# Kernel optimization log

Measured on AMD Instinct MI355X. Metric: run time of the kernel, lower is better.

The kernel has to match this reference:

```python
import jax, jax.numpy as jnp
import numpy as np

N = 100000      # nodes
E = 3200000     # edges
H = 64          # node_hidden_dim
DIN = 15        # node_input_dim
DOUT = 12       # output_dim
NT = 5          # num_edge_type
G = 256         # graphs in batch
STEPS = 6       # num_step_prop


def setup_inputs() -> dict:
    key = jax.random.key(0)
    ks = jax.random.split(key, 24)
    s = 0.1
    n = lambda k, shp: jax.random.normal(k, shp, jnp.float32) * s
    return {
        "x": jax.random.normal(ks[0], (N, DIN), jnp.float32),
        "edge_index": jax.random.randint(ks[1], (2, E), 0, N, dtype=jnp.int32),
        "edge_attr": jax.random.randint(ks[2], (E,), 0, NT, dtype=jnp.int32),
        "batch": jnp.sort(jax.random.randint(ks[3], (N,), 0, G, dtype=jnp.int32)),
        "lin0_w": n(ks[4], (DIN, H)), "lin0_b": n(ks[5], (H,)),
        "edge_embed": n(ks[6], (NT, H * H)),
        "conv_bias": n(ks[7], (H,)),
        "gru_w_ih": n(ks[8], (H, 3 * H)), "gru_w_hh": n(ks[9], (H, 3 * H)),
        "gru_b_ih": n(ks[10], (3 * H,)), "gru_b_hh": n(ks[11], (3 * H,)),
        "i_w1": n(ks[12], (2 * H, H)), "i_b1": n(ks[13], (H,)),
        "i_w2": n(ks[14], (H, DOUT)), "i_b2": n(ks[15], (DOUT,)),
        "j_w1": n(ks[16], (H, H)), "j_b1": n(ks[17], (H,)),
        "j_w2": n(ks[18], (H, DOUT)), "j_b2": n(ks[19], (DOUT,)),
    }


def reference(x, edge_index, edge_attr, batch,
              lin0_w, lin0_b, edge_embed, conv_bias,
              gru_w_ih, gru_w_hh, gru_b_ih, gru_b_hh,
              i_w1, i_b1, i_w2, i_b2, j_w1, j_b1, j_w2, j_b2):
    src, dst = edge_index[0], edge_index[1]
    W_types = edge_embed.reshape(NT, H, H)  # per edge-type [H_in, H_out]

    # in-degree for mean aggregation (PyG: isolated nodes get 0)
    deg = jax.ops.segment_sum(jnp.ones((E,), x.dtype), dst, num_segments=N)
    deg = jnp.maximum(deg, 1.0)[:, None]

    out0 = jax.nn.relu(x @ lin0_w + lin0_b)
    out = out0
    h = out0

    for _ in range(STEPS):
        # NNConv: per-edge matmul m_e = x_src[e] @ W[type_e].
        # Only NT=5 edge types exist -> precompute all 5 transforms, then gather.
        T = jnp.einsum('nh,tho->nto', out, W_types)        # [N, NT, H]
        msg = T[src, edge_attr]                            # [E, H] gather
        agg = jax.ops.segment_sum(msg, dst, num_segments=N) / deg + conv_bias
        m = jax.nn.relu(agg)

        # GRU cell (torch gate order: r, z, n)
        gx = m @ gru_w_ih + gru_b_ih
        gh = h @ gru_w_hh + gru_b_hh
        xr, xz, xn = jnp.split(gx, 3, axis=1)
        hr, hz, hn = jnp.split(gh, 3, axis=1)
        r = jax.nn.sigmoid(xr + hr)
        z = jax.nn.sigmoid(xz + hz)
        nn_ = jnp.tanh(xn + r * hn)
        h = (1.0 - z) * nn_ + z * h
        out = h

    # gated readout
    i = jax.nn.sigmoid(
        jax.nn.sigmoid(jnp.concatenate([out, out0], axis=1) @ i_w1 + i_b1) @ i_w2 + i_b2)
    j = jax.nn.sigmoid(out @ j_w1 + j_b1) @ j_w2 + j_b2
    gated = i * j                                          # [N, DOUT]
    return jax.ops.segment_sum(gated, batch, num_segments=G)  # [G, DOUT]
```

## Files before the change

kernel.cpp:

```cpp
#include <hip/hip_runtime.h>
#include <hip/hip_bf16.h>

typedef __hip_bfloat16 bf16;
using short8 = __attribute__((ext_vector_type(8))) short;
using f32x4  = __attribute__((ext_vector_type(4))) float;
using f32x2  = __attribute__((ext_vector_type(2))) float;

#define MFMA16(a,b,c) __builtin_amdgcn_mfma_f32_16x16x32_bf16((a),(b),(c),0,0,0)
#define MAXBUCK 4096
#define SB 72
#define MSTR 72
#define SRCCAP 1024
#define CHK 8192
#define MAXNC 512
#define BCAP 2816

__device__ __forceinline__ float b2f(bf16 v){ return __bfloat162float(v); }
__device__ __forceinline__ bf16  f2b(float v){ return __float2bfloat16(v); }
__device__ __forceinline__ float sigmf(float x){ return 1.f/(1.f+__expf(-x)); }
__device__ __forceinline__ float tanhfast(float x){
  x = fminf(fmaxf(x,-15.f),15.f);
  float e = __expf(2.f*x);
  return (e-1.f)/(e+1.f);
}
__device__ __forceinline__ short8 ld_frag(const bf16* p){
  return *reinterpret_cast<const short8*>(p);
}
__device__ __forceinline__ short f2bits(float f){
  unsigned u = __builtin_bit_cast(unsigned, f);
  unsigned r = (u + 0x7FFFu + ((u>>16)&1u)) >> 16;
  return (short)r;
}
__device__ __forceinline__ f32x2 pk_add(f32x2 a, f32x2 b){
  f32x2 d;
  asm("v_pk_add_f32 %0, %1, %2" : "=v"(d) : "v"(a), "v"(b));
  return d;
}
__device__ __forceinline__ unsigned cvtpk_bf16(float lo, float hi){
  unsigned r;
  asm("v_cvt_pk_bf16_f32 %0, %1, %2" : "=v"(r) : "v"(lo), "v"(hi));
  return r;
}

__device__ __forceinline__ f32x2 cvt8lo(unsigned w){
  f32x2 r;
  asm("v_cvt_pk_f32_fp8 %0, %1" : "=v"(r) : "v"(w));
  return r;
}
__device__ __forceinline__ f32x2 cvt8hi(unsigned w){
  return cvt8lo(w >> 16);
}
__device__ __forceinline__ unsigned short f32pair_to_fp8(float a, float b){
  unsigned r = 0;
  asm("v_cvt_pk_fp8_f32 %0, %1, %2" : "+v"(r) : "v"(a), "v"(b));
  return (unsigned short)(r & 0xffffu);
}

__global__ void k_sniff(const unsigned int* __restrict__ x, int* __restrict__ flag,
      int* __restrict__ bkt_cnt, int nb,
      int* __restrict__ s0, int* __restrict__ s1,
      int* __restrict__ s2, int* __restrict__ s3){
  int t = threadIdx.x;
  if (blockIdx.x == 1){
    for (int i=t;i<nb;i+=256) bkt_cnt[i]=0;
    return;
  }
  if (blockIdx.x == 2){
    if (t<32){ s0[t]=0; s1[t]=0; }
    if (t<16){ s2[t]=0; s3[t]=0; }
    return;
  }
  int good = 0;
  for (int i=t; i<4096; i+=256){
    unsigned w = x[i];
    unsigned e = (w>>23)&0xFFu;
    unsigned m = w & 0x7FFFFFFFu;
    if ((e>=100u && e<=150u) || m==0u) good++;
  }
  __shared__ int sm[256];
  sm[t]=good; __syncthreads();
  if (t==0){ int s=0; for (int k=0;k<256;k++) s+=sm[k]; *flag = (s>2048)?1:0; }
}

struct PtrPack { const void* p[17]; };

#define CAN_X     0
#define CAN_L0W   1500032
#define CAN_L0B   1500992
#define CAN_EE    1501056
#define CAN_CB    1521536
#define CAN_WIH   1521600
#define CAN_WHH   1533888
#define CAN_BIH   1546176
#define CAN_BHH   1546368
#define CAN_IW1   1546560
#define CAN_IB1   1554752
#define CAN_IW2   1554816
#define CAN_IB2   1555584
#define CAN_JW1   1555648
#define CAN_JB1   1559744
#define CAN_JW2   1559808
#define CAN_JB2   1560576
#define CAN_TOT   1560640

__global__ void k_canon(PtrPack pk, const int* __restrict__ flag, bf16* __restrict__ dst){
  static const int offs[17] = {CAN_X,CAN_L0W,CAN_L0B,CAN_EE,CAN_CB,CAN_WIH,CAN_WHH,
    CAN_BIH,CAN_BHH,CAN_IW1,CAN_IB1,CAN_IW2,CAN_IB2,CAN_JW1,CAN_JB1,CAN_JW2,CAN_JB2};
  static const int szs[17]  = {1500000,960,64,20480,64,12288,12288,192,192,8192,64,768,12,4096,64,768,12};
  int t = blockIdx.x*256+threadIdx.x;
  if (t >= CAN_TOT) return;
  int s = 0;
  #pragma unroll
  for (int k=1;k<17;k++) if (t >= offs[k]) s = k;
  int i = t - offs[s];
  float v = 0.f;
  if (i < szs[s]){
    if (*flag) v = ((const float*)pk.p[s])[i];
    else       v = b2f(((const bf16*)pk.p[s])[i]);
  }
  dst[t] = f2b(v);
}


__global__ __launch_bounds__(1024) void k_scan(const int* __restrict__ cnt, int n,
      int* __restrict__ ptr, int* __restrict__ cursor){
  __shared__ int ws[17];
  int tid = threadIdx.x, lane = tid&63, w = tid>>6;
  int run = 0;
  for (int base=0; base<n; base+=1024){
    int i = base + tid;
    int v = (i<n)? cnt[i] : 0;
    int incl = v;
    #pragma unroll
    for (int off=1; off<64; off<<=1){
      int t = __shfl_up(incl, off, 64);
      if (lane>=off) incl += t;
    }
    if (lane==63) ws[w] = incl;
    __syncthreads();
    if (tid==0){ int r=0; for (int k=0;k<16;k++){ int t=ws[k]; ws[k]=r; r+=t; } ws[16]=r; }
    __syncthreads();
    int excl = run + ws[w] + incl - v;
    if (i<n){
      ptr[i] = excl;
      if (cursor) cursor[i] = excl;
    }
    run += ws[16];
    __syncthreads();
  }
  if (tid==0) ptr[n] = run;
}

__global__ __launch_bounds__(512) void k_csort(const int* __restrict__ srcv,
      const int* __restrict__ dstv, const int* __restrict__ eav, int E_, int nb, int NC,
      unsigned int* __restrict__ bucketed, int* __restrict__ rs, int* __restrict__ bkt_cnt){
  __shared__ int lh[MAXBUCK];
  __shared__ int lofs[MAXBUCK];
  __shared__ int ws[9];
  int c = blockIdx.x, tid = threadIdx.x;
  int base = c*CHK, end = min(base+CHK, E_);
  for (int i=tid;i<nb;i+=512) lh[i]=0;
  __syncthreads();
  for (int i=base+tid; i<end; i+=512) atomicAdd(&lh[dstv[i]>>5], 1);
  __syncthreads();
  int lane=tid&63, w=tid>>6;
  int run=0;
  for (int bb=0; bb<nb; bb+=512){
    int i=bb+tid;
    int v=(i<nb)? lh[i]:0;
    int incl=v;
    #pragma unroll
    for (int off=1;off<64;off<<=1){
      int t=__shfl_up(incl,off,64);
      if (lane>=off) incl+=t;
    }
    if (lane==63) ws[w]=incl;
    __syncthreads();
    if (tid==0){ int r=0; for(int k=0;k<8;k++){int t=ws[k];ws[k]=r;r+=t;} ws[8]=r; }
    __syncthreads();
    if (i<nb) lofs[i]= run + ws[w] + incl - v;
    run += ws[8];
    __syncthreads();
  }
  for (int i=tid;i<nb;i+=512){
    rs[(size_t)i*NC + c] = base + lofs[i];
    int cntv = lh[i];
    if (cntv) atomicAdd(&bkt_cnt[i], cntv);
  }
  if (tid==0) rs[(size_t)nb*NC + c] = end;
  __syncthreads();
  for (int i=base+tid;i<end;i+=512){
    int d = dstv[i];
    int bin = d>>5;
    int pos = base + atomicAdd(&lofs[bin], 1);
    bucketed[pos] = (((unsigned)((d&31)*5 + eav[i]))<<17) | (unsigned)srcv[i];
  }
}

__global__ __launch_bounds__(256) void k_bsort2(const unsigned int* __restrict__ bucketed,
      const int* __restrict__ rs, int NC,
      const int* __restrict__ bkt_ptr, int nb, int E_,
      int* __restrict__ kptr, int* __restrict__ sorted_src,
      unsigned char* __restrict__ kperm){
  __shared__ unsigned sbuf[BCAP];
  __shared__ int rofs[MAXNC+1];
  __shared__ int rstart[MAXNC];
  __shared__ int scan2[2][MAXNC];
  __shared__ int cnt[160], sc[160], cur[160];
  int b = blockIdx.x, tid = threadIdx.x;
  int s = bkt_ptr[b], e = bkt_ptr[b+1];
  int size = e - s;
  const int* rowA = rs + (size_t)b*NC;
  const int* rowB = rs + (size_t)(b+1)*NC;
  bool fits = (NC <= MAXNC);
  if (fits){
    for (int i=tid; i<MAXNC; i+=256){
      int v = 0;
      if (i < NC){
        int a = rowA[i];
        rstart[i] = a;
        v = rowB[i] - a;
      }
      scan2[0][i] = v;
    }
    __syncthreads();
    int pp = 0;
    #pragma unroll
    for (int off=1; off<MAXNC; off<<=1){
      for (int i=tid; i<MAXNC; i+=256){
        int nv = scan2[pp][i];
        if (i>=off) nv += scan2[pp][i-off];
        scan2[pp^1][i] = nv;
      }
      __syncthreads();
      pp ^= 1;
    }
    if (tid==0) rofs[0]=0;
    for (int i=tid; i<NC; i+=256) rofs[i+1] = scan2[pp][i];
    __syncthreads();
  }
  bool staged = fits && (size <= BCAP);
  if (staged){
    for (int i=tid; i<size; i+=256){
      int lo=0, hi=NC-1;
      while (lo<hi){ int mid=(lo+hi+1)>>1; if (rofs[mid]<=i) lo=mid; else hi=mid-1; }
      sbuf[i] = bucketed[rstart[lo] + (i - rofs[lo])];
    }
  }
  __syncthreads();
  if (tid<160) cnt[tid]=0;
  __syncthreads();
  if (staged){
    for (int i=tid;i<size;i+=256) atomicAdd(&cnt[sbuf[i]>>17], 1);
  } else {
    for (int c2=0;c2<NC;c2++){
      int st=rowA[c2], ln=rowB[c2]-st;
      for (int k=tid;k<ln;k+=256) atomicAdd(&cnt[bucketed[st+k]>>17], 1);
    }
  }
  __syncthreads();
  if (tid<160) sc[tid]=cnt[tid];
  __syncthreads();
  #pragma unroll
  for (int off=1; off<160; off<<=1){
    int v = 0;
    if (tid<160 && tid>=off) v = sc[tid-off];
    __syncthreads();
    if (tid<160) sc[tid] += v;
    __syncthreads();
  }
  if (tid<160){
    int basek = s + sc[tid] - cnt[tid];
    kptr[b*160+tid] = basek;
    cur[tid] = basek;
  }
  if (b==nb-1 && tid==0) kptr[(size_t)nb*160] = e;
  if (tid<160){
    int hbase = (tid<80)? 0 : 80;
    int me = cnt[tid];
    int r = 0;
    for (int j=0;j<80;j++){
      int jj = hbase+j;
      int cj = cnt[jj];
      r += (cj>me) || (cj==me && jj<tid);
    }
    kperm[((size_t)b*2 + (tid<80?0:1))*80 + r] = (unsigned char)(tid - hbase);
  }
  __syncthreads();
  if (staged){
    for (int i=tid;i<size;i+=256){
      unsigned p = sbuf[i];
      int pos = atomicAdd(&cur[p>>17], 1);
      sorted_src[pos] = (int)(p & 0x1FFFFu);
    }
  } else {
    for (int c2=0;c2<NC;c2++){
      int st=rowA[c2], ln=rowB[c2]-st;
      for (int k=tid;k<ln;k+=256){
        unsigned p = bucketed[st+k];
        int pos = atomicAdd(&cur[p>>17], 1);
        sorted_src[pos] = (int)(p & 0x1FFFFu);
      }
    }
  }
}

__global__ __launch_bounds__(256) void k_lin0(const bf16* __restrict__ x,
      const bf16* __restrict__ w, const bf16* __restrict__ b,
      bf16* __restrict__ out0, bf16* __restrict__ h,
      unsigned char* __restrict__ hq, int N_){
  int idx = blockIdx.x*256+threadIdx.x;
  int n = idx>>6, o = idx&63;
  if (n>=N_) return;
  float acc = b2f(b[o]);
  #pragma unroll
  for (int k=0;k<15;k++) acc += b2f(x[n*15+k]) * b2f(w[k*64+o]);
  float hv = fmaxf(acc,0.f);
  bf16 v = f2b(hv);
  out0[idx]=v; h[idx]=v;
  float hvn = __shfl_xor(hv, 1);
  if (!(o&1)) *(unsigned short*)(hq + (size_t)n*64 + o) = f32pair_to_fp8(hv, hvn);
}

__device__ __forceinline__ void d_swz(const unsigned short* src, int KS, int NC,
                                      unsigned short* dst, int nfrag, int t){
  if (t >= nfrag*64) return;
  int lane=t&63, frag=t>>6, cb=frag/KS, ks=frag%KS;
  int c = cb*16 + (lane&15);
  #pragma unroll
  for (int j=0;j<8;j++){
    int k = ks*32 + ((lane>>4)<<3) + j;
    dst[t*8+j] = (c<NC)? src[k*NC+c] : (unsigned short)0;
  }
}

__global__ __launch_bounds__(256) void k_prep(const bf16* __restrict__ ee,
      const bf16* __restrict__ wih, const bf16* __restrict__ whh,
      const bf16* __restrict__ iw1, const bf16* __restrict__ jw1,
      const bf16* __restrict__ iw2, const bf16* __restrict__ jw2,
      unsigned short* __restrict__ wall, unsigned short* __restrict__ wgru,
      unsigned short* __restrict__ wr1, unsigned short* __restrict__ wiw2s,
      unsigned short* __restrict__ wjw2s,
      const int* __restrict__ batch, int N_, int G_, int* __restrict__ gptr){
  int blk = blockIdx.x, tid = threadIdx.x;
  if (blk < 10){
    int t = blk*256+tid;
    if (t<2560){
      int lane=t&63, frag=t>>6, ct=frag/10, ks=frag%10;
      int c = ct*16 + (lane&15);
      #pragma unroll
      for (int j=0;j<8;j++){
        int k = ks*32 + ((lane>>4)<<3) + j;
        int tt = k>>6, kc = k&63;
        wall[t*8+j] = ((const unsigned short*)ee)[tt*4096 + kc*64 + c];
      }
    }
  } else if (blk < 16){
    d_swz((const unsigned short*)wih, 2, 192, wgru, 24, (blk-10)*256+tid);
  } else if (blk < 22){
    d_swz((const unsigned short*)whh, 2, 192, wgru+12288, 24, (blk-16)*256+tid);
  } else if (blk < 26){
    d_swz((const unsigned short*)iw1, 4, 64, wr1, 16, (blk-22)*256+tid);
  } else if (blk < 28){
    d_swz((const unsigned short*)jw1, 2, 64, wr1+8192, 8, (blk-26)*256+tid);
  } else if (blk == 28){
    d_swz((const unsigned short*)iw2, 2, 12, wiw2s, 2, tid);
  } else if (blk == 29){
    d_swz((const unsigned short*)jw2, 2, 12, wjw2s, 2, tid);
  } else {
    int g = (blk-30)*256+tid;
    if (g <= G_){
      int lo=0, hi=N_;
      while (lo<hi){ int mid=(lo+hi)>>1; if (batch[mid] < g) lo=mid+1; else hi=mid; }
      gptr[g]=lo;
    }
  }
}

__global__ __launch_bounds__(256,8) void k_step(const bf16* __restrict__ hin,
      bf16* __restrict__ hout,
      const unsigned char* __restrict__ hqin, unsigned char* __restrict__ hqout,
      const int* __restrict__ sorted_src, const int* __restrict__ kptr,
      const unsigned char* __restrict__ kperm,
      const unsigned short* __restrict__ wall, const unsigned short* __restrict__ wgru,
      const bf16* __restrict__ conv_bias, const bf16* __restrict__ bih,
      const bf16* __restrict__ bhh, int N_){
  __shared__ unsigned short Sb[80*SB];
  __shared__ int kp[81];
  __shared__ unsigned char pm[80];
  __shared__ char ubuf[SRCCAP*4 + 32];
  int* srcL = (int*)ubuf;
  unsigned short* m_s = (unsigned short*)ubuf;
  int tid=threadIdx.x, lane=tid&63, w=tid>>6;
  int b=blockIdx.x;
  if (tid<81) kp[tid]=kptr[(size_t)b*80+tid];
  if (tid<80) pm[tid]=kperm[(size_t)b*80+tid];
  __syncthreads();
  int s0g = kp[0];
  int elen = kp[80]-s0g;
  int cap = (elen<=SRCCAP)? elen : 0;
  for (int i=tid;i<cap;i+=256) srcL[i]=sorted_src[s0g+i]<<6;
  __syncthreads();
  int g=lane>>3, c=lane&7;
  const unsigned char* hp8 = hqin + (c<<3);
  const int sent = N_<<6;

  auto run_phase1 = [&](auto GET){
    #pragma unroll 1
    for (int jo=0;jo<5;jo++){
      int pbase = jo*16 + w*4;
      int p  = pm[pbase + (g&3)];
      int p0 = pm[pbase];
      int st = kp[p]-s0g, len = kp[p+1]-kp[p];
      int maxLen = kp[p0+1]-kp[p0];
      int sub = g>>2;
      f32x2 a01={0.f,0.f}, a23={0.f,0.f}, a45={0.f,0.f}, a67={0.f,0.f};
      for (int base=0; base<maxLen; base+=8){
        uint2 hv[4];
        #pragma unroll
        for (int u=0;u<4;u++){
          int idx = base + sub*4 + u;
          int s = GET(st+idx);
          s = (idx < len)? s : sent;
          hv[u] = *(const uint2*)(hp8 + (size_t)s);
        }
        #pragma unroll
        for (int u=0;u<4;u++){
          a01 = pk_add(a01, cvt8lo(hv[u].x));
          a23 = pk_add(a23, cvt8hi(hv[u].x));
          a45 = pk_add(a45, cvt8lo(hv[u].y));
          a67 = pk_add(a67, cvt8hi(hv[u].y));
        }
      }
      float a[8] = {a01.x,a01.y,a23.x,a23.y,a45.x,a45.y,a67.x,a67.y};
      #pragma unroll
      for (int j=0;j<8;j++) a[j] += __shfl_xor(a[j], 32);
      if (g<4){
        uint4 v;
        v.x = cvtpk_bf16(a[0],a[1]);
        v.y = cvtpk_bf16(a[2],a[3]);
        v.z = cvtpk_bf16(a[4],a[5]);
        v.w = cvtpk_bf16(a[6],a[7]);
        *reinterpret_cast<uint4*>(&Sb[(size_t)p*SB + c*8]) = v;
      }
    }
  };
  if (cap) run_phase1([&](int rel){ return srcL[rel]; });
  else     run_phase1([&](int rel){ return sorted_src[s0g+rel]<<6; });
  __syncthreads();

  int q=lane>>4, mr=lane&15;
  {
    int ct = w;
    f32x4 acc={0.f,0.f,0.f,0.f};
    #pragma unroll
    for (int ks=0;ks<10;ks++){
      int k0 = ks*32 + q*8;
      int tt = k0>>6, ch = k0&63;
      short8 af = *reinterpret_cast<const short8*>(&Sb[(size_t)(mr*5+tt)*SB + ch]);
      short8 bfrag = *(const short8*)(wall + (size_t)((ct*10+ks)*64+lane)*8);
      acc = MFMA16(af, bfrag, acc);
    }
    int col = ct*16+mr;
    float bi = b2f(conv_bias[col]);
    #pragma unroll
    for (int r=0;r<4;r++){
      int nl = q*4+r;
      int deg = kp[nl*5+5]-kp[nl*5];
      float dv = 1.f/fmaxf((float)deg,1.f);
      m_s[nl*MSTR+col] = (unsigned short)f2bits(fmaxf(acc[r]*dv+bi,0.f));
    }
  }
  __syncthreads();

  {
    int cc = w;
    int na = b*16+mr; if (na>N_-1) na=N_-1;
    short8 am0 = *(const short8*)(&m_s[mr*MSTR + q*8]);
    short8 am1 = *(const short8*)(&m_s[mr*MSTR + 32 + q*8]);
    short8 ah0 = ld_frag(hin + (size_t)na*64 + q*8);
    short8 ah1 = ld_frag(hin + (size_t)na*64 + 32 + q*8);
    const short8* Bw = reinterpret_cast<const short8*>(wgru);
    f32x4 xr={0.f,0.f,0.f,0.f}, xz=xr, xn=xr, hr=xr, hz=xr, hn=xr;
    xr = MFMA16(am0, Bw[((cc  )*2+0)*64+lane], xr);
    xr = MFMA16(am1, Bw[((cc  )*2+1)*64+lane], xr);
    xz = MFMA16(am0, Bw[((cc+4)*2+0)*64+lane], xz);
    xz = MFMA16(am1, Bw[((cc+4)*2+1)*64+lane], xz);
    xn = MFMA16(am0, Bw[((cc+8)*2+0)*64+lane], xn);
    xn = MFMA16(am1, Bw[((cc+8)*2+1)*64+lane], xn);
    hr = MFMA16(ah0, Bw[(24+(cc  )*2+0)*64+lane], hr);
    hr = MFMA16(ah1, Bw[(24+(cc  )*2+1)*64+lane], hr);
    hz = MFMA16(ah0, Bw[(24+(cc+4)*2+0)*64+lane], hz);
    hz = MFMA16(ah1, Bw[(24+(cc+4)*2+1)*64+lane], hz);
    hn = MFMA16(ah0, Bw[(24+(cc+8)*2+0)*64+lane], hn);
    hn = MFMA16(ah1, Bw[(24+(cc+8)*2+1)*64+lane], hn);
    int col = cc*16+mr;
    float bxr=b2f(bih[col]), bxz=b2f(bih[col+64]), bxn=b2f(bih[col+128]);
    float bhr=b2f(bhh[col]), bhz=b2f(bhh[col+64]), bhn=b2f(bhh[col+128]);
    #pragma unroll
    for (int r=0;r<4;r++){
      int row = q*4+r;
      int n = b*16+row;
      int nc = (n<N_)? n : N_-1;
      float rg = sigmf(xr[r]+bxr + hr[r]+bhr);
      float zg = sigmf(xz[r]+bxz + hz[r]+bhz);
      float ng = tanhfast(xn[r]+bxn + rg*(hn[r]+bhn));
      float ho = b2f(hin[(size_t)nc*64+col]);
      float hv = (1.f-zg)*ng + zg*ho;
      float hvn = __shfl_xor(hv, 1);
      if (n < N_){
        hout[(size_t)n*64+col] = f2b(hv);
        if (!(mr&1))
          *(unsigned short*)(hqout + (size_t)n*64 + col) = f32pair_to_fp8(hv, hvn);
      }
    }
  }
}

__global__ __launch_bounds__(256) void k_read(const bf16* __restrict__ h, const bf16* __restrict__ out0,
      const unsigned short* __restrict__ W, const bf16* __restrict__ ib1, const bf16* __restrict__ jb1,
      const unsigned short* __restrict__ iw2swz, const unsigned short* __restrict__ jw2swz,
      const bf16* __restrict__ ib2, const bf16* __restrict__ jb2,
      float* __restrict__ gated, int N_){
  __shared__ unsigned short lds[12288];
  __shared__ unsigned short sbuf[64*72];
  __shared__ unsigned short tbuf[64*72];
  { const int* s=(const int*)W; int* d=(int*)lds;
    for (int i=threadIdx.x;i<6144;i+=256) d[i]=s[i]; }
  __syncthreads();
  int tid=threadIdx.x, lane=tid&63, w=tid>>6, q=lane>>4;
  int nb = blockIdx.x*64 + w*16;
  int ar = nb + (lane&15); if (ar>N_-1) ar=N_-1;
  short8 ah0 = ld_frag(h + (size_t)ar*64 + q*8),    ah1 = ld_frag(h + (size_t)ar*64 + 32 + q*8);
  short8 ao0 = ld_frag(out0 + (size_t)ar*64 + q*8), ao1 = ld_frag(out0 + (size_t)ar*64 + 32 + q*8);
  const short8* Bi = reinterpret_cast<const short8*>(lds);
  const short8* Bj = reinterpret_cast<const short8*>(lds + 8192);
  int colb = lane&15;
  for (int cb=0; cb<4; cb++){
    f32x4 ai = {0.f,0.f,0.f,0.f};
    ai = MFMA16(ah0, Bi[(cb*4+0)*64+lane], ai);
    ai = MFMA16(ah1, Bi[(cb*4+1)*64+lane], ai);
    ai = MFMA16(ao0, Bi[(cb*4+2)*64+lane], ai);
    ai = MFMA16(ao1, Bi[(cb*4+3)*64+lane], ai);
    f32x4 aj = {0.f,0.f,0.f,0.f};
    aj = MFMA16(ah0, Bj[(cb*2+0)*64+lane], aj);
    aj = MFMA16(ah1, Bj[(cb*2+1)*64+lane], aj);
    int col = cb*16 + colb;
    float bi=b2f(ib1[col]), bj=b2f(jb1[col]);
    #pragma unroll
    for (int r=0;r<4;r++){
      int lrow = w*16 + q*4 + r;
      sbuf[lrow*72+col] = (unsigned short)f2bits(sigmf(ai[r]+bi));
      tbuf[lrow*72+col] = (unsigned short)f2bits(sigmf(aj[r]+bj));
    }
  }
  __syncthreads();
  int mr = lane&15;
  short8 as0 = *(const short8*)(&sbuf[(w*16+mr)*72 + q*8]);
  short8 as1 = *(const short8*)(&sbuf[(w*16+mr)*72 + 32 + q*8]);
  short8 at0 = *(const short8*)(&tbuf[(w*16+mr)*72 + q*8]);
  short8 at1 = *(const short8*)(&tbuf[(w*16+mr)*72 + 32 + q*8]);
  const short8* Bi2 = reinterpret_cast<const short8*>(iw2swz);
  const short8* Bj2 = reinterpret_cast<const short8*>(jw2swz);
  f32x4 ai = {0.f,0.f,0.f,0.f};
  ai = MFMA16(as0, Bi2[lane], ai);
  ai = MFMA16(as1, Bi2[64+lane], ai);
  f32x4 aj = {0.f,0.f,0.f,0.f};
  aj = MFMA16(at0, Bj2[lane], aj);
  aj = MFMA16(at1, Bj2[64+lane], aj);
  int col = lane&15;
  if (col<12){
    float bi=b2f(ib2[col]), bj=b2f(jb2[col]);
    #pragma unroll
    for (int r=0;r<4;r++){
      int row = nb + q*4 + r;
      if (row < N_) gated[(size_t)row*12+col] = sigmf(ai[r]+bi)*(aj[r]+bj);
    }
  }
}

__global__ __launch_bounds__(256) void k_graphsum(const float* __restrict__ gated,
      const int* __restrict__ gptr, const int* __restrict__ flag, void* __restrict__ outp){
  int g = blockIdx.x;
  int s = gptr[g], e = gptr[g+1];
  int tid = threadIdx.x;
  int c = tid & 15, rg = tid >> 4;
  float acc = 0.f;
  if (c < 12)
    for (int row = s + rg; row < e; row += 16) acc += gated[(size_t)row*12 + c];
  __shared__ float sm[256];
  sm[tid] = acc;
  __syncthreads();
  if (rg == 0 && c < 12){
    float t = 0.f;
    for (int k=0;k<16;k++) t += sm[k*16 + c];
    if (*flag) ((float*)outp)[g*12 + c] = t;
    else       ((bf16*) outp)[g*12 + c] = f2b(t);
  }
}


extern "C" void kernel_launch(void* const* d_in, const int* in_sizes, int n_in,
                              void* d_out, int out_size, void* d_ws, size_t ws_size,
                              hipStream_t stream){
  const int*  ei    = (const int*) d_in[1];
  const int*  ea    = (const int*) d_in[2];
  const int*  batch = (const int*) d_in[3];

  const int N_ = in_sizes[3];
  const int E_ = in_sizes[2];
  const int G_ = out_size / 12;
  const int nb  = (N_ + 31) >> 5;
  const int nbs = (N_ + 15) >> 4;
  const int NC  = (E_ + CHK - 1) / CHK;

  char* ws = (char*)d_ws;
  size_t off = 0;
  auto alloc = [&](size_t bytes)->size_t{
    size_t o = off; off += (bytes + 255) & ~(size_t)255; return o;
  };

  size_t oOut0   = alloc((size_t)N_*64*2);
  size_t oH0     = alloc((size_t)(N_+1)*64*2);
  size_t oH1     = alloc((size_t)(N_+1)*64*2);
  size_t oHq0    = alloc((size_t)(N_+1)*64);
  size_t oHq1    = alloc((size_t)(N_+1)*64);
  size_t oGated  = alloc((size_t)N_*12*4);
  size_t oBEdges = alloc((size_t)E_*4);
  size_t oSorted = alloc((size_t)E_*4 + 256);
  size_t oRS     = alloc((size_t)(nb+1)*NC*4);
  size_t oKptr   = alloc(((size_t)nb*160+2)*4);
  size_t oKperm  = alloc((size_t)nb*160);
  size_t oCanon  = alloc((size_t)CAN_TOT*2);
  size_t oCnt    = alloc((size_t)nb*4);
  size_t oBPtr   = alloc((size_t)(nb+1)*4);
  size_t oGptr   = alloc((size_t)(G_+1)*4);
  size_t oFlag   = alloc(256);
  size_t oWall   = alloc((size_t)20480*2);
  size_t oWgru   = alloc((size_t)24576*2);
  size_t oWr1    = alloc((size_t)12288*2);
  size_t oWiw2   = alloc((size_t)1024*2);
  size_t oWjw2   = alloc((size_t)1024*2);

  bf16*  out0    = (bf16*)(ws + oOut0);
  bf16*  h0      = (bf16*)(ws + oH0);
  bf16*  h1      = (bf16*)(ws + oH1);
  unsigned char* hq0 = (unsigned char*)(ws + oHq0);
  unsigned char* hq1 = (unsigned char*)(ws + oHq1);
  float* gated   = (float*)(ws + oGated);
  unsigned int* bucketed = (unsigned int*)(ws + oBEdges);
  int*   sorted_src = (int*)(ws + oSorted);
  int*   rs      = (int*)(ws + oRS);
  int*   kptr    = (int*)(ws + oKptr);
  unsigned char* kperm = (unsigned char*)(ws + oKperm);
  bf16*  can     = (bf16*)(ws + oCanon);
  int*   bkt_cnt = (int*)(ws + oCnt);
  int*   bkt_ptr = (int*)(ws + oBPtr);
  int*   gptr    = (int*)(ws + oGptr);
  int*   flag    = (int*)(ws + oFlag);
  unsigned short* wall  = (unsigned short*)(ws + oWall);
  unsigned short* wgru  = (unsigned short*)(ws + oWgru);
  unsigned short* wr1   = (unsigned short*)(ws + oWr1);
  unsigned short* wiw2s = (unsigned short*)(ws + oWiw2);
  unsigned short* wjw2s = (unsigned short*)(ws + oWjw2);

  const bf16* xC    = can + CAN_X;
  const bf16* l0wC  = can + CAN_L0W;
  const bf16* l0bC  = can + CAN_L0B;
  const bf16* eeC   = can + CAN_EE;
  const bf16* cbC   = can + CAN_CB;
  const bf16* wihC  = can + CAN_WIH;
  const bf16* whhC  = can + CAN_WHH;
  const bf16* bihC  = can + CAN_BIH;
  const bf16* bhhC  = can + CAN_BHH;
  const bf16* iw1C  = can + CAN_IW1;
  const bf16* ib1C  = can + CAN_IB1;
  const bf16* iw2C  = can + CAN_IW2;
  const bf16* ib2C  = can + CAN_IB2;
  const bf16* jw1C  = can + CAN_JW1;
  const bf16* jb1C  = can + CAN_JB1;
  const bf16* jw2C  = can + CAN_JW2;
  const bf16* jb2C  = can + CAN_JB2;

  PtrPack pk;
  pk.p[0]=d_in[0];  pk.p[1]=d_in[4];  pk.p[2]=d_in[5];  pk.p[3]=d_in[6];
  pk.p[4]=d_in[7];  pk.p[5]=d_in[8];  pk.p[6]=d_in[9];  pk.p[7]=d_in[10];
  pk.p[8]=d_in[11]; pk.p[9]=d_in[12]; pk.p[10]=d_in[13]; pk.p[11]=d_in[14];
  pk.p[12]=d_in[15]; pk.p[13]=d_in[16]; pk.p[14]=d_in[17]; pk.p[15]=d_in[18];
  pk.p[16]=d_in[19];

  const int gNw  = (N_+63)/64;

  k_sniff<<<3, 256, 0, stream>>>((const unsigned int*)d_in[0], flag,
                                 bkt_cnt, nb,
                                 (int*)(ws + oH0 + (size_t)N_*128),
                                 (int*)(ws + oH1 + (size_t)N_*128),
                                 (int*)(ws + oHq0 + (size_t)N_*64),
                                 (int*)(ws + oHq1 + (size_t)N_*64));
  k_canon<<<(CAN_TOT+255)/256, 256, 0, stream>>>(pk, flag, can);
  k_csort<<<NC, 512, 0, stream>>>(ei, ei + E_, ea, E_, nb, NC, bucketed, rs, bkt_cnt);
  k_scan<<<1, 1024, 0, stream>>>(bkt_cnt, nb, bkt_ptr, nullptr);
  k_bsort2<<<nb, 256, 0, stream>>>(bucketed, rs, NC, bkt_ptr, nb, E_, kptr, sorted_src, kperm);
  k_lin0<<<(N_*64+255)/256, 256, 0, stream>>>(xC, l0wC, l0bC, out0, h0, hq0, N_);
  k_prep<<<32, 256, 0, stream>>>(eeC, wihC, whhC, iw1C, jw1C, iw2C, jw2C,
                                 wall, wgru, wr1, wiw2s, wjw2s, batch, N_, G_, gptr);

  bf16* hb[2] = {h0, h1};
  unsigned char* hqb[2] = {hq0, hq1};
  for (int step = 0; step < 6; ++step){
    k_step<<<nbs, 256, 0, stream>>>(hb[step&1], hb[(step+1)&1],
                                    hqb[step&1], hqb[(step+1)&1],
                                    sorted_src, kptr, kperm,
                                    wall, wgru, cbC, bihC, bhhC, N_);
  }
  bf16* hfin = hb[0];

  k_read<<<gNw, 256, 0, stream>>>(hfin, out0, wr1, ib1C, jb1C, wiw2s, wjw2s,
                                  ib2C, jb2C, gated, N_);
  k_graphsum<<<G_, 256, 0, stream>>>(gated, gptr, flag, d_out);
}
```

Before: 657.1 us.

## Drop scan and graphsum kernels; fuse graph reduction via atomics and prefix into bsort

Removes the single-block scan kernel: each bucket-sort block now computes its own start offset by reducing all preceding bucket counts. Replaces the per-node gated buffer and graph-sum kernel with atomic accumulation into a small per-graph buffer inside the readout kernel, followed by a tiny finalize kernel. It also pre-shifts source indices by 6 when writing sorted_src, so the step kernel skips that shift on every load. This cuts kernel launches and a large intermediate write/read, at the cost of redundant prefix work per block, heavy atomic contention on few addresses, and a float summation order that is no longer deterministic.

```diff
diff --git a/kernel.cpp b/kernel.cpp
--- a/kernel.cpp
+++ b/kernel.cpp
@@ -59,7 +59,8 @@
 __global__ void k_sniff(const unsigned int* __restrict__ x, int* __restrict__ flag,
       int* __restrict__ bkt_cnt, int nb,
       int* __restrict__ s0, int* __restrict__ s1,
-      int* __restrict__ s2, int* __restrict__ s3){
+      int* __restrict__ s2, int* __restrict__ s3,
+      float* __restrict__ gatedG, int ng12){
   int t = threadIdx.x;
   if (blockIdx.x == 1){
     for (int i=t;i<nb;i+=256) bkt_cnt[i]=0;
@@ -68,6 +69,7 @@
   if (blockIdx.x == 2){
     if (t<32){ s0[t]=0; s1[t]=0; }
     if (t<16){ s2[t]=0; s3[t]=0; }
+    for (int i=t;i<ng12;i+=256) gatedG[i]=0.f;
     return;
   }
   int good = 0;
@@ -122,35 +124,6 @@
 }
 
 
-__global__ __launch_bounds__(1024) void k_scan(const int* __restrict__ cnt, int n,
-      int* __restrict__ ptr, int* __restrict__ cursor){
-  __shared__ int ws[17];
-  int tid = threadIdx.x, lane = tid&63, w = tid>>6;
-  int run = 0;
-  for (int base=0; base<n; base+=1024){
-    int i = base + tid;
-    int v = (i<n)? cnt[i] : 0;
-    int incl = v;
-    #pragma unroll
-    for (int off=1; off<64; off<<=1){
-      int t = __shfl_up(incl, off, 64);
-      if (lane>=off) incl += t;
-    }
-    if (lane==63) ws[w] = incl;
-    __syncthreads();
-    if (tid==0){ int r=0; for (int k=0;k<16;k++){ int t=ws[k]; ws[k]=r; r+=t; } ws[16]=r; }
-    __syncthreads();
-    int excl = run + ws[w] + incl - v;
-    if (i<n){
-      ptr[i] = excl;
-      if (cursor) cursor[i] = excl;
-    }
-    run += ws[16];
-    __syncthreads();
-  }
-  if (tid==0) ptr[n] = run;
-}
-
 __global__ __launch_bounds__(512) void k_csort(const int* __restrict__ srcv,
       const int* __restrict__ dstv, const int* __restrict__ eav, int E_, int nb, int NC,
       unsigned int* __restrict__ bucketed, int* __restrict__ rs, int* __restrict__ bkt_cnt){
@@ -199,7 +172,7 @@
 
 __global__ __launch_bounds__(256) void k_bsort2(const unsigned int* __restrict__ bucketed,
       const int* __restrict__ rs, int NC,
-      const int* __restrict__ bkt_ptr, int nb, int E_,
+      const int* __restrict__ bkt_cnt, int nb, int E_,
       int* __restrict__ kptr, int* __restrict__ sorted_src,
       unsigned char* __restrict__ kperm){
   __shared__ unsigned sbuf[BCAP];
@@ -207,8 +180,22 @@
   __shared__ int rstart[MAXNC];
   __shared__ int scan2[2][MAXNC];
   __shared__ int cnt[160], sc[160], cur[160];
+  __shared__ int red[256];
+  __shared__ int sE[2];
   int b = blockIdx.x, tid = threadIdx.x;
-  int s = bkt_ptr[b], e = bkt_ptr[b+1];
+  {
+    int acc=0;
+    for (int i=tid;i<b;i+=256) acc += bkt_cnt[i];
+    red[tid]=acc; __syncthreads();
+    #pragma unroll
+    for (int off=128; off>0; off>>=1){
+      if (tid<off) red[tid]+=red[tid+off];
+      __syncthreads();
+    }
+    if (tid==0){ sE[0]=red[0]; sE[1]=red[0]+bkt_cnt[b]; }
+    __syncthreads();
+  }
+  int s = sE[0], e = sE[1];
   int size = e - s;
   const int* rowA = rs + (size_t)b*NC;
   const int* rowB = rs + (size_t)(b+1)*NC;
@@ -291,7 +278,7 @@
     for (int i=tid;i<size;i+=256){
       unsigned p = sbuf[i];
       int pos = atomicAdd(&cur[p>>17], 1);
-      sorted_src[pos] = (int)(p & 0x1FFFFu);
+      sorted_src[pos] = (int)((p & 0x1FFFFu)<<6);
     }
   } else {
     for (int c2=0;c2<NC;c2++){
@@ -299,7 +286,7 @@
       for (int k=tid;k<ln;k+=256){
         unsigned p = bucketed[st+k];
         int pos = atomicAdd(&cur[p>>17], 1);
-        sorted_src[pos] = (int)(p & 0x1FFFFu);
+        sorted_src[pos] = (int)((p & 0x1FFFFu)<<6);
       }
     }
   }
@@ -399,7 +386,7 @@
   int s0g = kp[0];
   int elen = kp[80]-s0g;
   int cap = (elen<=SRCCAP)? elen : 0;
-  for (int i=tid;i<cap;i+=256) srcL[i]=sorted_src[s0g+i]<<6;
+  for (int i=tid;i<cap;i+=256) srcL[i]=sorted_src[s0g+i];
   __syncthreads();
   int g=lane>>3, c=lane&7;
   const unsigned char* hp8 = hqin + (c<<3);
@@ -446,7 +433,7 @@
     }
   };
   if (cap) run_phase1([&](int rel){ return srcL[rel]; });
-  else     run_phase1([&](int rel){ return sorted_src[s0g+rel]<<6; });
+  else     run_phase1([&](int rel){ return sorted_src[s0g+rel]; });
   __syncthreads();
 
   int q=lane>>4, mr=lane&15;
@@ -521,7 +508,7 @@
       const unsigned short* __restrict__ W, const bf16* __restrict__ ib1, const bf16* __restrict__ jb1,
       const unsigned short* __restrict__ iw2swz, const unsigned short* __restrict__ jw2swz,
       const bf16* __restrict__ ib2, const bf16* __restrict__ jb2,
-      float* __restrict__ gated, int N_){
+      const int* __restrict__ batch, float* __restrict__ gatedG, int N_){
   __shared__ unsigned short lds[12288];
   __shared__ unsigned short sbuf[64*72];
   __shared__ unsigned short tbuf[64*72];
@@ -574,28 +561,21 @@
     #pragma unroll
     for (int r=0;r<4;r++){
       int row = nb + q*4 + r;
-      if (row < N_) gated[(size_t)row*12+col] = sigmf(ai[r]+bi)*(aj[r]+bj);
-    }
-  }
-}
-
-__global__ __launch_bounds__(256) void k_graphsum(const float* __restrict__ gated,
-      const int* __restrict__ gptr, const int* __restrict__ flag, void* __restrict__ outp){
-  int g = blockIdx.x;
-  int s = gptr[g], e = gptr[g+1];
-  int tid = threadIdx.x;
-  int c = tid & 15, rg = tid >> 4;
-  float acc = 0.f;
-  if (c < 12)
-    for (int row = s + rg; row < e; row += 16) acc += gated[(size_t)row*12 + c];
-  __shared__ float sm[256];
-  sm[tid] = acc;
-  __syncthreads();
-  if (rg == 0 && c < 12){
-    float t = 0.f;
-    for (int k=0;k<16;k++) t += sm[k*16 + c];
-    if (*flag) ((float*)outp)[g*12 + c] = t;
-    else       ((bf16*) outp)[g*12 + c] = f2b(t);
+      if (row < N_){
+        float val = sigmf(ai[r]+bi)*(aj[r]+bj);
+        atomicAdd(&gatedG[batch[row]*12+col], val);
+      }
+    }
+  }
+}
+
+__global__ __launch_bounds__(256) void k_fin(const float* __restrict__ gatedG,
+      const int* __restrict__ flag, void* __restrict__ outp, int ng12){
+  int f = *flag;
+  for (int i=threadIdx.x; i<ng12; i+=256){
+    float t = gatedG[i];
+    if (f) ((float*)outp)[i] = t;
+    else   ((bf16*) outp)[i] = f2b(t);
   }
 }
 
@@ -625,7 +605,7 @@
   size_t oH1     = alloc((size_t)(N_+1)*64*2);
   size_t oHq0    = alloc((size_t)(N_+1)*64);
   size_t oHq1    = alloc((size_t)(N_+1)*64);
-  size_t oGated  = alloc((size_t)N_*12*4);
+  size_t oGatedG = alloc((size_t)G_*12*4);
   size_t oBEdges = alloc((size_t)E_*4);
   size_t oSorted = alloc((size_t)E_*4 + 256);
   size_t oRS     = alloc((size_t)(nb+1)*NC*4);
@@ -633,7 +613,6 @@
   size_t oKperm  = alloc((size_t)nb*160);
   size_t oCanon  = alloc((size_t)CAN_TOT*2);
   size_t oCnt    = alloc((size_t)nb*4);
-  size_t oBPtr   = alloc((size_t)(nb+1)*4);
   size_t oGptr   = alloc((size_t)(G_+1)*4);
   size_t oFlag   = alloc(256);
   size_t oWall   = alloc((size_t)20480*2);
@@ -647,7 +626,7 @@
   bf16*  h1      = (bf16*)(ws + oH1);
   unsigned char* hq0 = (unsigned char*)(ws + oHq0);
   unsigned char* hq1 = (unsigned char*)(ws + oHq1);
-  float* gated   = (float*)(ws + oGated);
+  float* gatedG  = (float*)(ws + oGatedG);
   unsigned int* bucketed = (unsigned int*)(ws + oBEdges);
   int*   sorted_src = (int*)(ws + oSorted);
   int*   rs      = (int*)(ws + oRS);
@@ -655,7 +634,6 @@
   unsigned char* kperm = (unsigned char*)(ws + oKperm);
   bf16*  can     = (bf16*)(ws + oCanon);
   int*   bkt_cnt = (int*)(ws + oCnt);
-  int*   bkt_ptr = (int*)(ws + oBPtr);
   int*   gptr    = (int*)(ws + oGptr);
   int*   flag    = (int*)(ws + oFlag);
   unsigned short* wall  = (unsigned short*)(ws + oWall);
@@ -696,11 +674,11 @@
                                  (int*)(ws + oH0 + (size_t)N_*128),
                                  (int*)(ws + oH1 + (size_t)N_*128),
                                  (int*)(ws + oHq0 + (size_t)N_*64),
-                                 (int*)(ws + oHq1 + (size_t)N_*64));
+                                 (int*)(ws + oHq1 + (size_t)N_*64),
+                                 gatedG, G_*12);
   k_canon<<<(CAN_TOT+255)/256, 256, 0, stream>>>(pk, flag, can);
   k_csort<<<NC, 512, 0, stream>>>(ei, ei + E_, ea, E_, nb, NC, bucketed, rs, bkt_cnt);
-  k_scan<<<1, 1024, 0, stream>>>(bkt_cnt, nb, bkt_ptr, nullptr);
-  k_bsort2<<<nb, 256, 0, stream>>>(bucketed, rs, NC, bkt_ptr, nb, E_, kptr, sorted_src, kperm);
+  k_bsort2<<<nb, 256, 0, stream>>>(bucketed, rs, NC, bkt_cnt, nb, E_, kptr, sorted_src, kperm);
   k_lin0<<<(N_*64+255)/256, 256, 0, stream>>>(xC, l0wC, l0bC, out0, h0, hq0, N_);
   k_prep<<<32, 256, 0, stream>>>(eeC, wihC, whhC, iw1C, jw1C, iw2C, jw2C,
                                  wall, wgru, wr1, wiw2s, wjw2s, batch, N_, G_, gptr);
@@ -716,6 +694,6 @@
   bf16* hfin = hb[0];
 
   k_read<<<gNw, 256, 0, stream>>>(hfin, out0, wr1, ib1C, jb1C, wiw2s, wjw2s,
-                                  ib2C, jb2C, gated, N_);
-  k_graphsum<<<G_, 256, 0, stream>>>(gated, gptr, flag, d_out);
-}
+                                  ib2C, jb2C, batch, gatedG, N_);
+  k_fin<<<1, 256, 0, stream>>>(gatedG, flag, d_out, G_*12);
+}
```

New measurement: 745.3 us. 13.4% more time.
